# Kernel tuning notes

Measured on AMD Instinct MI355X. Metric: run time of the kernel, lower is better.

The kernel has to match this reference:

```python
import jax, jax.numpy as jnp
import numpy as np

EMBED_DIM = 1024
NUM_HEADS = 16
D_K = EMBED_DIM // NUM_HEADS
MAX_SEQ = 2048
BATCH = 2
SEQ = 2048
ROPE_BASE = 10000.0


def build_rope(seq_len, head_dim, base=ROPE_BASE):
    # standard RoPE: inv_freq over half the head dim, cos/sin of shape [seq, head_dim]
    inv_freq = 1.0 / (base ** (jnp.arange(0, head_dim, 2, dtype=jnp.float32) / head_dim))
    t = jnp.arange(seq_len, dtype=jnp.float32)
    freqs = jnp.einsum('s,d->sd', t, inv_freq)              # [S, D/2]
    emb = jnp.concatenate([freqs, freqs], axis=-1)          # [S, D]
    return jnp.cos(emb), jnp.sin(emb)


def rotate_half(x):
    x1, x2 = jnp.split(x, 2, axis=-1)
    return jnp.concatenate([-x2, x1], axis=-1)


def apply_rope(x, cos, sin):
    # x: [B, H, S, D]; cos/sin: [S, D] -> broadcast over batch & heads
    cos = cos[None, None, :, :]
    sin = sin[None, None, :, :]
    return x * cos + rotate_half(x) * sin


def setup_inputs() -> dict:
    key = jax.random.key(0)
    ks = jax.random.split(key, 9)
    scale = 1.0 / np.sqrt(EMBED_DIM)
    x = jax.random.normal(ks[0], (BATCH, SEQ, EMBED_DIM), dtype=jnp.float32)
    # causal boolean mask, broadcastable to [B, H, S, S]
    mask = jnp.tril(jnp.ones((SEQ, SEQ), dtype=bool))[None, None, :, :]
    cos, sin = build_rope(MAX_SEQ, D_K)
    Wq = jax.random.normal(ks[1], (EMBED_DIM, EMBED_DIM), jnp.float32) * scale
    bq = jnp.zeros((EMBED_DIM,), jnp.float32)
    Wk = jax.random.normal(ks[2], (EMBED_DIM, EMBED_DIM), jnp.float32) * scale
    bk = jnp.zeros((EMBED_DIM,), jnp.float32)
    Wv = jax.random.normal(ks[3], (EMBED_DIM, EMBED_DIM), jnp.float32) * scale
    bv = jnp.zeros((EMBED_DIM,), jnp.float32)
    Wo = jax.random.normal(ks[4], (EMBED_DIM, EMBED_DIM), jnp.float32) * scale
    bo = jnp.zeros((EMBED_DIM,), jnp.float32)
    return {'x': x, 'mask': mask, 'cos': cos, 'sin': sin,
            'Wq': Wq, 'bq': bq, 'Wk': Wk, 'bk': bk, 'Wv': Wv, 'bv': bv,
            'Wo': Wo, 'bo': bo}


def reference(x, mask, cos, sin, Wq, bq, Wk, bk, Wv, bv, Wo, bo):
    B, S, E = x.shape
    H, D = NUM_HEADS, D_K
    # nn.Linear: y = x @ W^T + b
    q = (x @ Wq.T + bq).reshape(B, S, H, D).transpose(0, 2, 1, 3)  # [B,H,S,D]
    k = (x @ Wk.T + bk).reshape(B, S, H, D).transpose(0, 2, 1, 3)
    v = (x @ Wv.T + bv).reshape(B, S, H, D).transpose(0, 2, 1, 3)
    q = apply_rope(q, cos[:S], sin[:S])
    k = apply_rope(k, cos[:S], sin[:S])
    scores = jnp.einsum('bhqd,bhkd->bhqk', q, k) / jnp.sqrt(jnp.float32(D))
    scores = jnp.where(mask, scores, -jnp.inf)
    attn = jax.nn.softmax(scores, axis=-1)
    out = jnp.einsum('bhqk,bhkd->bhqd', attn, v)
    out = out.transpose(0, 2, 1, 3).reshape(B, S, E)
    return out @ Wo.T + bo
```

## Files before the change

kernel.cpp:

```cpp
#include <hip/hip_runtime.h>
#include <hip/hip_bf16.h>
#include <cfloat>
#include <math.h>

#define EMBED 1024
#define NHEADS 16
#define DK 64
#define SEQL 2048
#define BATCH 2
#define NTOK 4096


typedef __bf16 bf16x8 __attribute__((ext_vector_type(8)));
typedef float floatx4 __attribute__((ext_vector_type(4)));

__device__ __forceinline__ unsigned short f2bf(float f) {
    union { __hip_bfloat16 b; unsigned short u; } c;
    c.b = __float2bfloat16(f);
    return c.u;
}

__device__ __forceinline__ void async16(void* lds, const void* g) {
    __builtin_amdgcn_global_load_lds(
        (const __attribute__((address_space(1))) unsigned int*)g,
        (__attribute__((address_space(3))) unsigned int*)lds,
        16, 0, 0);
}

__global__ __launch_bounds__(256) void convert_pack(
    const float* __restrict__ x,  const float* __restrict__ Wq,
    const float* __restrict__ Wk, const float* __restrict__ Wv,
    const float* __restrict__ Wo,
    unsigned short* __restrict__ xb, unsigned short* __restrict__ Wqkv,
    unsigned short* __restrict__ Wob)
{
    const int XG = 1048576, WG = 262144;
    int g = blockIdx.x * 256 + threadIdx.x;
    const float4* s; ushort4* d;
    if (g < XG)               { s = (const float4*)x  + g;                d = (ushort4*)xb   + g; }
    else if (g < XG + WG)     { s = (const float4*)Wq + (g - XG);         d = (ushort4*)Wqkv + (g - XG); }
    else if (g < XG + 2 * WG) { s = (const float4*)Wk + (g - XG - WG);    d = (ushort4*)Wqkv + (g - XG); }
    else if (g < XG + 3 * WG) { s = (const float4*)Wv + (g - XG - 2*WG);  d = (ushort4*)Wqkv + (g - XG); }
    else                      { s = (const float4*)Wo + (g - XG - 3*WG);  d = (ushort4*)Wob  + (g - XG - 3*WG); }
    float4 v = *s;
    *d = (ushort4){f2bf(v.x), f2bf(v.y), f2bf(v.z), f2bf(v.w)};
}

__global__ __launch_bounds__(256, 4) void qkv_gemm(
    const unsigned short* __restrict__ xb, const unsigned short* __restrict__ Wqkv,
    const float* __restrict__ bq, const float* __restrict__ bk, const float* __restrict__ bv,
    const float* __restrict__ cosT, const float* __restrict__ sinT,
    unsigned short* __restrict__ Qg, unsigned short* __restrict__ Kg,
    unsigned short* __restrict__ Vt)
{
    __shared__ __align__(16) unsigned short SM[16384];
    unsigned short* As0 = SM;
    unsigned short* As1 = SM + 4096;
    unsigned short* Bs0 = SM + 8192;
    unsigned short* Bs1 = SM + 12288;

    const int t = threadIdx.x, lane = t & 63, w = t >> 6;
    const int quad = lane >> 4, lrow = lane & 15;
    const int wr = w >> 1, wc = w & 1;
    const int m0 = blockIdx.y * 128;
    const int n0 = blockIdx.x * 128;
    const int srow = lane >> 2;
    const int scol = (lane & 3) * 8;

    floatx4 acc[4][4];
    #pragma unroll
    for (int i = 0; i < 4; i++)
        #pragma unroll
        for (int j = 0; j < 4; j++) acc[i][j] = (floatx4){0.f,0.f,0.f,0.f};

    for (int k0 = 0; k0 < EMBED; k0 += 64) {
        __syncthreads();
        #pragma unroll
        for (int c = 0; c < 2; c++) {
            const unsigned short* as = xb
                + (size_t)(m0 + w * 32 + c * 16 + srow) * EMBED + k0 + scol;
            async16(&As0[(w * 32 + c * 16) * 32], as);
            async16(&As1[(w * 32 + c * 16) * 32], as + 32);
            const unsigned short* bs = Wqkv
                + (size_t)(n0 + w * 32 + c * 16 + srow) * EMBED + k0 + scol;
            async16(&Bs0[(w * 32 + c * 16) * 32], bs);
            async16(&Bs1[(w * 32 + c * 16) * 32], bs + 32);
        }
        __syncthreads();

        #pragma unroll
        for (int ks = 0; ks < 2; ks++) {
            const unsigned short* Ab = ks ? As1 : As0;
            const unsigned short* Bb = ks ? Bs1 : Bs0;
            bf16x8 bfB[4];
            #pragma unroll
            for (int j = 0; j < 4; j++)
                bfB[j] = *reinterpret_cast<const bf16x8*>(
                    &Bb[(wc * 64 + j * 16 + lrow) * 32 + quad * 8]);
            #pragma unroll
            for (int i = 0; i < 4; i++) {
                bf16x8 af = *reinterpret_cast<const bf16x8*>(
                    &Ab[(wr * 64 + i * 16 + lrow) * 32 + quad * 8]);
                #pragma unroll
                for (int j = 0; j < 4; j++)
                    acc[i][j] = __builtin_amdgcn_mfma_f32_16x16x32_bf16(af, bfB[j], acc[i][j], 0, 0, 0);
            }
        }
    }

    const int mat   = n0 >> 10;
    const int nloc  = n0 & 1023;
    const int hbase = nloc >> 6;
    const int bb    = m0 >> 11;
    const int s0    = m0 & (SEQL - 1);

    if (mat == 2) {
        unsigned short* T2 = SM;
        #pragma unroll
        for (int hh = 0; hh < 2; hh++) {
            __syncthreads();
            if (wc == hh) {
                #pragma unroll
                for (int j = 0; j < 4; j++) {
                    int d = j * 16 + lrow;
                    float bvv = bv[nloc + hh * 64 + d];
                    #pragma unroll
                    for (int i = 0; i < 4; i++) {
                        int tok = wr * 64 + i * 16 + quad * 4;
                        *(ushort4*)&T2[d * 136 + tok] = (ushort4){
                            f2bf(acc[i][j][0] + bvv), f2bf(acc[i][j][1] + bvv),
                            f2bf(acc[i][j][2] + bvv), f2bf(acc[i][j][3] + bvv)};
                    }
                }
            }
            __syncthreads();
            int d = t >> 2, tg = (t & 3) * 32;
            unsigned short* dst = Vt
                + ((size_t)(bb * NHEADS + hbase + hh) * DK + d) * SEQL + s0 + tg;
            #pragma unroll
            for (int c = 0; c < 32; c += 8)
                *(uint4*)(dst + c) = *(const uint4*)&T2[d * 136 + tg + c];
        }
    } else {
        unsigned short* T = SM;
        const float* bias = (mat == 0) ? bq : bk;
        unsigned short* Og = (mat == 0) ? Qg : Kg;
        #pragma unroll
        for (int hh = 0; hh < 2; hh++) {
            __syncthreads();
            if (wc == hh) {
                #pragma unroll
                for (int j = 0; j < 4; j++) {
                    int d = j * 16 + lrow;
                    float cb = bias[nloc + hh * 64 + d];
                    float pb = bias[nloc + hh * 64 + (d ^ 32)];
                    float sgn = (d < 32) ? -1.0f : 1.0f;
                    #pragma unroll
                    for (int i = 0; i < 4; i++)
                        #pragma unroll
                        for (int rg = 0; rg < 4; rg++) {
                            int tok = wr * 64 + i * 16 + quad * 4 + rg;
                            int s = s0 + tok;
                            float cv = cosT[s * DK + d];
                            float sv = sinT[s * DK + d];
                            float val = (acc[i][j][rg] + cb) * cv
                                      + sgn * (acc[i][j ^ 2][rg] + pb) * sv;
                            T[tok * 72 + d] = f2bf(val);
                        }
                }
            }
            __syncthreads();
            int tok = t >> 1, dh = (t & 1) * 32;
            unsigned short* dst = Og
                + ((size_t)(bb * NHEADS + hbase + hh) * SEQL + s0 + tok) * DK + dh;
            #pragma unroll
            for (int c = 0; c < 32; c += 8)
                *(uint4*)(dst + c) = *(const uint4*)&T[tok * 72 + dh + c];
        }
    }
}

#define KP 72

__global__ __launch_bounds__(256) void attn_mfma(
    const unsigned short* __restrict__ Qg, const unsigned short* __restrict__ Kg,
    const unsigned short* __restrict__ Vt, unsigned short* __restrict__ CTX)
{
    __shared__ __align__(16) unsigned short Ks[64 * KP];
    __shared__ __align__(16) unsigned short Vs[64 * KP];
    __shared__ __align__(16) unsigned short Ps[64 * KP];

    const int QT_MAX = SEQL / 64 - 1;
    const int qt = (blockIdx.y & 8) ? blockIdx.x : (QT_MAX - blockIdx.x);
    const int h = blockIdx.y, b = blockIdx.z;
    const int t = threadIdx.x;
    const int lane = t & 63, w = t >> 6;
    const int quad = lane >> 4, lrow = lane & 15;
    const int q0 = qt * 64;

    const unsigned short* Qh = Qg + (size_t)(b * NHEADS + h) * SEQL * DK;
    const unsigned short* Kh = Kg + (size_t)(b * NHEADS + h) * SEQL * DK;
    const unsigned short* Vh = Vt + (size_t)(b * NHEADS + h) * DK * SEQL;

    bf16x8 aq[2];
    #pragma unroll
    for (int ks = 0; ks < 2; ks++)
        aq[ks] = *(const bf16x8*)(Qh + (size_t)(q0 + w * 16 + lrow) * DK + quad * 8 + ks * 32);

    floatx4 of[4];
    float l[4] = {0,0,0,0};
    #pragma unroll
    for (int jd = 0; jd < 4; jd++) of[jd] = (floatx4){0,0,0,0};

    unsigned short* Pw = Ps + w * 16 * KP;

    const int r0 = t >> 3, c8 = (t & 7) * 8;
    uint4 pk0, pk1, pv0, pv1;
    auto pref = [&](int k0) {
        pk0 = *(const uint4*)(Kh + (size_t)(k0 + r0) * DK + c8);
        pk1 = *(const uint4*)(Kh + (size_t)(k0 + r0 + 32) * DK + c8);
        pv0 = *(const uint4*)(Vh + (size_t)r0 * SEQL + k0 + c8);
        pv1 = *(const uint4*)(Vh + (size_t)(r0 + 32) * SEQL + k0 + c8);
    };
    pref(0);

    for (int kt = 0; kt <= qt; kt++) {
        const int k0 = kt * 64;
        __syncthreads();
        *(uint4*)&Ks[r0 * KP + c8]        = pk0;
        *(uint4*)&Ks[(r0 + 32) * KP + c8] = pk1;
        *(uint4*)&Vs[r0 * KP + c8]        = pv0;
        *(uint4*)&Vs[(r0 + 32) * KP + c8] = pv1;
        __syncthreads();
        if (kt < qt) pref(k0 + 64);

        floatx4 sc[4];
        #pragma unroll
        for (int j = 0; j < 4; j++) sc[j] = (floatx4){0,0,0,0};
        #pragma unroll
        for (int ks = 0; ks < 2; ks++)
            #pragma unroll
            for (int j = 0; j < 4; j++) {
                bf16x8 kb = *reinterpret_cast<const bf16x8*>(&Ks[(j * 16 + lrow) * KP + quad * 8 + ks * 32]);
                sc[j] = __builtin_amdgcn_mfma_f32_16x16x32_bf16(aq[ks], kb, sc[j], 0, 0, 0);
            }

        const bool diag = (kt == qt);
        #pragma unroll
        for (int rg = 0; rg < 4; rg++) {
            int row = q0 + w * 16 + quad * 4 + rg;
            float lacc = 0.f;
            #pragma unroll
            for (int j = 0; j < 4; j++) {
                float pval = __expf(sc[j][rg] * 0.125f);
                if (diag && (k0 + j * 16 + lrow) > row) pval = 0.f;
                Pw[(quad * 4 + rg) * KP + j * 16 + lrow] = f2bf(pval);
                lacc += pval;
            }
            l[rg] += lacc;
        }
        #pragma unroll
        for (int ks = 0; ks < 2; ks++) {
            bf16x8 pa = *reinterpret_cast<const bf16x8*>(&Pw[lrow * KP + quad * 8 + ks * 32]);
            #pragma unroll
            for (int jd = 0; jd < 4; jd++) {
                bf16x8 vb = *reinterpret_cast<const bf16x8*>(&Vs[(jd * 16 + lrow) * KP + quad * 8 + ks * 32]);
                of[jd] = __builtin_amdgcn_mfma_f32_16x16x32_bf16(pa, vb, of[jd], 0, 0, 0);
            }
        }
    }

    #pragma unroll
    for (int rg = 0; rg < 4; rg++) {
        float lv = l[rg];
        #pragma unroll
        for (int off = 1; off < 16; off <<= 1) lv += __shfl_xor(lv, off);
        float inv = 1.0f / lv;
        int row = q0 + w * 16 + quad * 4 + rg;
        unsigned short* Cr = CTX + ((size_t)(b * NHEADS + h) * SEQL + row) * DK;
        #pragma unroll
        for (int jd = 0; jd < 4; jd++) Cr[jd * 16 + lrow] = f2bf(of[jd][rg] * inv);
    }
}

__global__ __launch_bounds__(256) void o_gemm(
    const unsigned short* __restrict__ Ag,
    const unsigned short* __restrict__ Bg,
    const float* __restrict__ bias, float* __restrict__ C)
{
    __shared__ __align__(16) unsigned short SM[12288];
    unsigned short* As0 = SM;
    unsigned short* As1 = SM + 4096;
    unsigned short* Bs0 = SM + 8192;
    unsigned short* Bs1 = SM + 10240;

    const int t = threadIdx.x, lane = t & 63, wave = t >> 6;
    const int quad = lane >> 4, lrow = lane & 15;
    const int m0 = blockIdx.y * 128, n0 = blockIdx.x * 64;
    const int srow = lane >> 2;
    const int scol = (lane & 3) * 8;

    floatx4 acc[2][4];
    #pragma unroll
    for (int i = 0; i < 2; i++)
        #pragma unroll
        for (int j = 0; j < 4; j++) acc[i][j] = (floatx4){0.f,0.f,0.f,0.f};

    for (int k0 = 0; k0 < EMBED; k0 += 64) {
        const int hh = k0 >> 6;
        __syncthreads();
        #pragma unroll
        for (int c = 0; c < 2; c++) {
            int tok = m0 + wave * 32 + c * 16 + srow;
            const unsigned short* as = Ag
                + ((size_t)((tok >> 11) * NHEADS + hh) * SEQL + (tok & (SEQL - 1))) * DK + scol;
            async16(&As0[wave * 1024 + c * 512], as);
            async16(&As1[wave * 1024 + c * 512], as + 32);
        }
        const unsigned short* bs = Bg + (size_t)(n0 + wave * 16 + srow) * EMBED + k0 + scol;
        async16(&Bs0[wave * 512], bs);
        async16(&Bs1[wave * 512], bs + 32);
        __syncthreads();

        #pragma unroll
        for (int ks = 0; ks < 2; ks++) {
            const unsigned short* Ab = ks ? As1 : As0;
            const unsigned short* Bb = ks ? Bs1 : Bs0;
            bf16x8 af[2], bfB[4];
            #pragma unroll
            for (int i = 0; i < 2; i++)
                af[i] = *reinterpret_cast<const bf16x8*>(&Ab[(wave * 32 + i * 16 + lrow) * 32 + quad * 8]);
            #pragma unroll
            for (int j = 0; j < 4; j++)
                bfB[j] = *reinterpret_cast<const bf16x8*>(&Bb[(j * 16 + lrow) * 32 + quad * 8]);
            #pragma unroll
            for (int i = 0; i < 2; i++)
                #pragma unroll
                for (int j = 0; j < 4; j++)
                    acc[i][j] = __builtin_amdgcn_mfma_f32_16x16x32_bf16(af[i], bfB[j], acc[i][j], 0, 0, 0);
        }
    }

    #pragma unroll
    for (int i = 0; i < 2; i++)
        #pragma unroll
        for (int rg = 0; rg < 4; rg++) {
            int row_g = m0 + wave * 32 + i * 16 + quad * 4 + rg;
            #pragma unroll
            for (int j = 0; j < 4; j++) {
                int col_g = n0 + j * 16 + lrow;
                C[(size_t)row_g * EMBED + col_g] = acc[i][j][rg] + bias[col_g];
            }
        }
}

extern "C" void kernel_launch(void* const* d_in, const int* in_sizes, int n_in,
                              void* d_out, int out_size, void* d_ws, size_t ws_size,
                              hipStream_t stream) {
    const float* x    = (const float*)d_in[0];
    const float* cosT = (const float*)d_in[2];
    const float* sinT = (const float*)d_in[3];
    const float* Wq = (const float*)d_in[4];  const float* bq = (const float*)d_in[5];
    const float* Wk = (const float*)d_in[6];  const float* bk = (const float*)d_in[7];
    const float* Wv = (const float*)d_in[8];  const float* bv = (const float*)d_in[9];
    const float* Wo = (const float*)d_in[10]; const float* bo = (const float*)d_in[11];

    const size_t MB = 1024 * 1024;
    char* ws = (char*)d_ws;
    unsigned short* xb   = (unsigned short*)(ws);
    unsigned short* Wqkv = (unsigned short*)(ws +  8 * MB);
    unsigned short* Wob  = (unsigned short*)(ws + 14 * MB);
    unsigned short* Qg   = (unsigned short*)(ws + 16 * MB);
    unsigned short* Kg   = (unsigned short*)(ws + 24 * MB);
    unsigned short* Vt   = (unsigned short*)(ws + 32 * MB);
    unsigned short* CTXb = (unsigned short*)(ws + 40 * MB);

    convert_pack<<<8192, 256, 0, stream>>>(x, Wq, Wk, Wv, Wo, xb, Wqkv, Wob);

    dim3 qkv_grid(3 * EMBED / 128, NTOK / 128);
    qkv_gemm<<<qkv_grid, 256, 0, stream>>>(xb, Wqkv, bq, bk, bv, cosT, sinT, Qg, Kg, Vt);

    dim3 attn_grid(SEQL / 64, NHEADS, BATCH);
    attn_mfma<<<attn_grid, 256, 0, stream>>>(Qg, Kg, Vt, CTXb);

    dim3 o_grid(EMBED / 64, NTOK / 128);
    o_gemm<<<o_grid, 256, 0, stream>>>(CTXb, Wob, bo, (float*)d_out);
}
```

Baseline: 214.0 us.

## Double-buffer K-chunk loads in QKV and output projection GEMMs

Both projection GEMMs are restructured so the K loop runs over 32-wide chunks that alternate between two LDS buffers. Each chunk's async global-to-LDS load is issued before the MFMA work on the previous chunk, so memory latency can overlap with compute. Before, each iteration loaded everything and then waited at a barrier before computing. The barrier count per K step stays about the same, and correctness relies on the barrier waiting for outstanding async LDS loads.

```diff
diff --git a/kernel.cpp b/kernel.cpp
--- a/kernel.cpp
+++ b/kernel.cpp
@@ -73,39 +73,42 @@
         #pragma unroll
         for (int j = 0; j < 4; j++) acc[i][j] = (floatx4){0.f,0.f,0.f,0.f};
 
-    for (int k0 = 0; k0 < EMBED; k0 += 64) {
-        __syncthreads();
-        #pragma unroll
-        for (int c = 0; c < 2; c++) {
-            const unsigned short* as = xb
-                + (size_t)(m0 + w * 32 + c * 16 + srow) * EMBED + k0 + scol;
-            async16(&As0[(w * 32 + c * 16) * 32], as);
-            async16(&As1[(w * 32 + c * 16) * 32], as + 32);
-            const unsigned short* bs = Wqkv
-                + (size_t)(n0 + w * 32 + c * 16 + srow) * EMBED + k0 + scol;
-            async16(&Bs0[(w * 32 + c * 16) * 32], bs);
-            async16(&Bs1[(w * 32 + c * 16) * 32], bs + 32);
-        }
-        __syncthreads();
-
-        #pragma unroll
-        for (int ks = 0; ks < 2; ks++) {
-            const unsigned short* Ab = ks ? As1 : As0;
-            const unsigned short* Bb = ks ? Bs1 : Bs0;
-            bf16x8 bfB[4];
+    auto stage = [&](int s) {
+        unsigned short* Ad = (s & 1) ? As1 : As0;
+        unsigned short* Bd = (s & 1) ? Bs1 : Bs0;
+        const unsigned short* as = xb
+            + (size_t)(m0 + w * 32 + srow) * EMBED + s * 32 + scol;
+        async16(&Ad[(w * 32) * 32],      as);
+        async16(&Ad[(w * 32 + 16) * 32], as + (size_t)16 * EMBED);
+        const unsigned short* bs = Wqkv
+            + (size_t)(n0 + w * 32 + srow) * EMBED + s * 32 + scol;
+        async16(&Bd[(w * 32) * 32],      bs);
+        async16(&Bd[(w * 32 + 16) * 32], bs + (size_t)16 * EMBED);
+    };
+    auto compute = [&](const unsigned short* Ab, const unsigned short* Bb) {
+        bf16x8 bfB[4];
+        #pragma unroll
+        for (int j = 0; j < 4; j++)
+            bfB[j] = *reinterpret_cast<const bf16x8*>(
+                &Bb[(wc * 64 + j * 16 + lrow) * 32 + quad * 8]);
+        #pragma unroll
+        for (int i = 0; i < 4; i++) {
+            bf16x8 af = *reinterpret_cast<const bf16x8*>(
+                &Ab[(wr * 64 + i * 16 + lrow) * 32 + quad * 8]);
             #pragma unroll
             for (int j = 0; j < 4; j++)
-                bfB[j] = *reinterpret_cast<const bf16x8*>(
-                    &Bb[(wc * 64 + j * 16 + lrow) * 32 + quad * 8]);
-            #pragma unroll
-            for (int i = 0; i < 4; i++) {
-                bf16x8 af = *reinterpret_cast<const bf16x8*>(
-                    &Ab[(wr * 64 + i * 16 + lrow) * 32 + quad * 8]);
-                #pragma unroll
-                for (int j = 0; j < 4; j++)
-                    acc[i][j] = __builtin_amdgcn_mfma_f32_16x16x32_bf16(af, bfB[j], acc[i][j], 0, 0, 0);
-            }
-        }
+                acc[i][j] = __builtin_amdgcn_mfma_f32_16x16x32_bf16(af, bfB[j], acc[i][j], 0, 0, 0);
+        }
+    };
+
+    stage(0);
+    for (int s = 0; s < 32; s += 2) {
+        __syncthreads();
+        if (s + 1 < 32) stage(s + 1);
+        compute(As0, Bs0);
+        __syncthreads();
+        if (s + 2 < 32) stage(s + 2);
+        compute(As1, Bs1);
     }
 
     const int mat   = n0 >> 10;
@@ -306,39 +309,44 @@
         #pragma unroll
         for (int j = 0; j < 4; j++) acc[i][j] = (floatx4){0.f,0.f,0.f,0.f};
 
-    for (int k0 = 0; k0 < EMBED; k0 += 64) {
-        const int hh = k0 >> 6;
-        __syncthreads();
+    auto stage = [&](int s) {
+        unsigned short* Ad = (s & 1) ? As1 : As0;
+        unsigned short* Bd = (s & 1) ? Bs1 : Bs0;
+        const int hh = s >> 1, dc = (s & 1) * 32;
         #pragma unroll
         for (int c = 0; c < 2; c++) {
             int tok = m0 + wave * 32 + c * 16 + srow;
             const unsigned short* as = Ag
-                + ((size_t)((tok >> 11) * NHEADS + hh) * SEQL + (tok & (SEQL - 1))) * DK + scol;
-            async16(&As0[wave * 1024 + c * 512], as);
-            async16(&As1[wave * 1024 + c * 512], as + 32);
-        }
-        const unsigned short* bs = Bg + (size_t)(n0 + wave * 16 + srow) * EMBED + k0 + scol;
-        async16(&Bs0[wave * 512], bs);
-        async16(&Bs1[wave * 512], bs + 32);
-        __syncthreads();
-
-        #pragma unroll
-        for (int ks = 0; ks < 2; ks++) {
-            const unsigned short* Ab = ks ? As1 : As0;
-            const unsigned short* Bb = ks ? Bs1 : Bs0;
-            bf16x8 af[2], bfB[4];
-            #pragma unroll
-            for (int i = 0; i < 2; i++)
-                af[i] = *reinterpret_cast<const bf16x8*>(&Ab[(wave * 32 + i * 16 + lrow) * 32 + quad * 8]);
+                + ((size_t)((tok >> 11) * NHEADS + hh) * SEQL + (tok & (SEQL - 1))) * DK + dc + scol;
+            async16(&Ad[(wave * 32 + c * 16) * 32], as);
+        }
+        const unsigned short* bs = Bg
+            + (size_t)(n0 + wave * 16 + srow) * EMBED + s * 32 + scol;
+        async16(&Bd[(wave * 16) * 32], bs);
+    };
+    auto compute = [&](const unsigned short* Ab, const unsigned short* Bb) {
+        bf16x8 af[2], bfB[4];
+        #pragma unroll
+        for (int i = 0; i < 2; i++)
+            af[i] = *reinterpret_cast<const bf16x8*>(&Ab[(wave * 32 + i * 16 + lrow) * 32 + quad * 8]);
+        #pragma unroll
+        for (int j = 0; j < 4; j++)
+            bfB[j] = *reinterpret_cast<const bf16x8*>(&Bb[(j * 16 + lrow) * 32 + quad * 8]);
+        #pragma unroll
+        for (int i = 0; i < 2; i++)
             #pragma unroll
             for (int j = 0; j < 4; j++)
-                bfB[j] = *reinterpret_cast<const bf16x8*>(&Bb[(j * 16 + lrow) * 32 + quad * 8]);
-            #pragma unroll
-            for (int i = 0; i < 2; i++)
-                #pragma unroll
-                for (int j = 0; j < 4; j++)
-                    acc[i][j] = __builtin_amdgcn_mfma_f32_16x16x32_bf16(af[i], bfB[j], acc[i][j], 0, 0, 0);
-        }
+                acc[i][j] = __builtin_amdgcn_mfma_f32_16x16x32_bf16(af[i], bfB[j], acc[i][j], 0, 0, 0);
+    };
+
+    stage(0);
+    for (int s = 0; s < 32; s += 2) {
+        __syncthreads();
+        if (s + 1 < 32) stage(s + 1);
+        compute(As0, Bs0);
+        __syncthreads();
+        if (s + 2 < 32) stage(s + 2);
+        compute(As1, Bs1);
     }
 
     #pragma unroll
```

Result: slower. 218.5 us (+2.1%).
